# Performance work log

Hardware: AMD Instinct MI355X
Metric: run time of the kernel (lower is better)

## Reference

```python
import jax, jax.numpy as jnp
import numpy as np

D = 64
NU = 30000
NI = 20000
LU = 50  # mailbox length at user nodes (item_max_length)
LI = 50  # mailbox length at item nodes (user_max_length)


def setup_inputs() -> dict:
    key = jax.random.key(0)
    ks = jax.random.split(key, 14)
    s = 0.05
    return {
        "user_feat": jax.random.normal(ks[0], (NU, D), jnp.float32),
        "item_feat": jax.random.normal(ks[1], (NI, D), jnp.float32),
        "W_u": jax.random.normal(ks[2], (D, D), jnp.float32) * s,
        "W_i": jax.random.normal(ks[3], (D, D), jnp.float32) * s,
        "Wg_u": jax.random.normal(ks[4], (2 * D, D), jnp.float32) * s,
        "Wg_i": jax.random.normal(ks[5], (2 * D, D), jnp.float32) * s,
        "i_te": jax.random.normal(ks[6], (LI, D), jnp.float32) * s,
        "i_te_k": jax.random.normal(ks[7], (LI, D), jnp.float32) * s,
        "u_te": jax.random.normal(ks[8], (LU, D), jnp.float32) * s,
        "u_te_k": jax.random.normal(ks[9], (LU, D), jnp.float32) * s,
        "item_nbr": jax.random.randint(ks[10], (NI, LI), 0, NU, jnp.int32),
        "item_time": jax.random.randint(ks[11], (NI, LI), 0, 1000000, jnp.int32),
        "user_nbr": jax.random.randint(ks[12], (NU, LU), 0, NI, jnp.int32),
        "user_time": jax.random.randint(ks[13], (NU, LU), 0, 1000000, jnp.int32),
    }


def _orgat_att(src_mb, dst_h, time, te, te_k):
    """One DGSR reduce: long-term time-encoded attention + short-term last-attention.
    src_mb: [N, L, d] gathered source features; dst_h: [N, d]; time: [N, L] int.
    Returns concat([h_long, h_short]) @ Wg applied by caller.
    """
    L = time.shape[1]
    d = src_mb.shape[-1]
    scale = jnp.sqrt(jnp.asarray(d, src_mb.dtype))
    # rank of each edge's time within the neighborhood; re_order: 0 = most recent
    rank = jnp.argsort(jnp.argsort(time, axis=1), axis=1)
    re_o = L - rank - 1                                       # [N, L]
    e = jnp.sum((te[re_o] + src_mb) * dst_h[:, None, :], axis=2) / scale
    alpha = jax.nn.softmax(e, axis=1)                         # [N, L]
    h_long = jnp.sum(alpha[..., None] * (src_mb + te_k[re_o]), axis=1)
    # short-term: attention keyed on the most-recent neighbor
    last = jnp.argmax(time, axis=1)
    last_em = jnp.take_along_axis(src_mb, last[:, None, None], axis=1)  # [N,1,d]
    e1 = jnp.sum(last_em * src_mb, axis=2) / scale
    a1 = jax.nn.softmax(e1, axis=1)
    h_short = jnp.sum(a1[..., None] * src_mb, axis=1)
    return jnp.concatenate([h_long, h_short], axis=-1)        # [N, 2d]


def reference(user_feat, item_feat, W_u, W_i, Wg_u, Wg_i, i_te, i_te_k,
              u_te, u_te_k, item_nbr, item_time, user_nbr, user_time):
    uh = user_feat @ W_u   # user_weight (feat_drop=0)
    ih = item_feat @ W_i   # item_weight
    # 'by' edges: users -> items (item reduce uses user mailboxes + i_time_encoding)
    u_mb = uh[item_nbr]                                        # [NI, LI, d]
    item_new = _orgat_att(u_mb, ih, item_time, i_te, i_te_k) @ Wg_i
    # 'pby' edges: items -> users (user reduce uses item mailboxes + u_time_encoding)
    i_mb = ih[user_nbr]                                        # [NU, LU, d]
    user_new = _orgat_att(i_mb, uh, user_time, u_te, u_te_k) @ Wg_u
    # residual update functions
    user_out = jax.nn.elu(user_new + user_feat)
    item_out = jax.nn.elu(item_new + item_feat)
    return user_out, item_out
```

## Files before the change

kernel.cpp:

```cpp
#include <hip/hip_runtime.h>
#include <stdint.h>

#define D   64
#define L   50
#define NUM_U 30000
#define NUM_I 20000
#define PW  1976


typedef __attribute__((ext_vector_type(8))) short short8x;
typedef __attribute__((ext_vector_type(4))) float f32x4;

__device__ __forceinline__ float lof(unsigned int u) {
    union { unsigned int i; float f; } v; v.i = u << 16; return v.f;
}
__device__ __forceinline__ float hif(unsigned int u) {
    union { unsigned int i; float f; } v; v.i = u & 0xffff0000u; return v.f;
}
__device__ __forceinline__ unsigned int f2bfbits(float f) {
    union { float f; unsigned int i; } v; v.f = f;
    return (v.i + 0x7fffu + ((v.i >> 16) & 1u)) >> 16;
}
__device__ __forceinline__ unsigned int packbf(float a, float b) {
    return f2bfbits(a) | (f2bfbits(b) << 16);
}
__device__ __forceinline__ float rl(float v, int l) {
    return __int_as_float(__builtin_amdgcn_readlane(__float_as_int(v), l));
}
__device__ __forceinline__ int rli(int v, int l) {
    return __builtin_amdgcn_readlane(v, l);
}

__global__ __launch_bounds__(256) void prep(
    const float* __restrict__ user_feat, const float* __restrict__ item_feat,
    const float* __restrict__ W_u, const float* __restrict__ W_i,
    const float* __restrict__ Wg_i, const float* __restrict__ Wg_u,
    const float* __restrict__ te_i, const float* __restrict__ te_u,
    const float* __restrict__ tk_i, const float* __restrict__ tk_u,
    unsigned int* __restrict__ H,
    unsigned short* __restrict__ WgPi, unsigned short* __restrict__ WgPu,
    unsigned short* __restrict__ tePi, unsigned short* __restrict__ tePu,
    unsigned short* __restrict__ tkPi, unsigned short* __restrict__ tkPu)
{
    const int tid = threadIdx.x;
    if (blockIdx.x < 3125) {
        const int lane = tid & 63, wid = tid >> 6;
        int r0 = blockIdx.x * 16 + wid * 4;
        const float* src; const float* W;
        if (r0 < NUM_U) { src = user_feat + (size_t)r0 * D;            W = W_u; }
        else            { src = item_feat + (size_t)(r0 - NUM_U) * D;  W = W_i; }
        float f0 = src[0 * D + lane], f1 = src[1 * D + lane];
        float f2 = src[2 * D + lane], f3 = src[3 * D + lane];
        float a0 = 0.f, a1 = 0.f, a2 = 0.f, a3 = 0.f;
#pragma unroll
        for (int k = 0; k < 64; k++) {
            float wk = W[k * 64 + lane];
            a0 += rl(f0, k) * wk; a1 += rl(f1, k) * wk;
            a2 += rl(f2, k) * wk; a3 += rl(f3, k) * wk;
        }
        int li = (lane & 31) << 1;
        float p0 = __shfl(a0, li), q0 = __shfl(a0, li | 1);
        float p1 = __shfl(a1, li), q1 = __shfl(a1, li | 1);
        float p2 = __shfl(a2, li), q2 = __shfl(a2, li | 1);
        float p3 = __shfl(a3, li), q3 = __shfl(a3, li | 1);
        if (lane < 32) {
            H[(size_t)(r0 + 0) * 32 + lane] = packbf(p0, q0);
            H[(size_t)(r0 + 1) * 32 + lane] = packbf(p1, q1);
            H[(size_t)(r0 + 2) * 32 + lane] = packbf(p2, q2);
            H[(size_t)(r0 + 3) * 32 + lane] = packbf(p3, q3);
        }
    } else {
        int gid = (blockIdx.x - 3125) * 256 + tid;
        for (int idx = gid; idx < 8192; idx += 4096) {
            int n = idx >> 7, k = idx & 127;
            WgPi[idx] = (unsigned short)f2bfbits(Wg_i[k * 64 + n]);
            WgPu[idx] = (unsigned short)f2bfbits(Wg_u[k * 64 + n]);
        }
        {
            int idx = gid;
            int r = idx >> 6, k = idx & 63;
            tePi[idx] = (r < L) ? (unsigned short)f2bfbits(te_i[r * 64 + k]) : 0;
            tePu[idx] = (r < L) ? (unsigned short)f2bfbits(te_u[r * 64 + k]) : 0;
            int d = idx >> 6, rr = idx & 63;
            tkPi[idx] = (rr < L) ? (unsigned short)f2bfbits(tk_i[rr * 64 + d]) : 0;
            tkPu[idx] = (rr < L) ? (unsigned short)f2bfbits(tk_u[rr * 64 + d]) : 0;
        }
    }
}

__global__ __launch_bounds__(256, 5) void attn_fused(
    const unsigned int* __restrict__ H,
    const float* __restrict__ user_feat, const float* __restrict__ item_feat,
    const unsigned short* __restrict__ WgPi, const unsigned short* __restrict__ WgPu,
    const unsigned short* __restrict__ tePi, const unsigned short* __restrict__ tePu,
    const unsigned short* __restrict__ tkPi, const unsigned short* __restrict__ tkPu,
    const int* __restrict__ item_nbr, const int* __restrict__ item_time,
    const int* __restrict__ user_nbr, const int* __restrict__ user_time,
    float* __restrict__ out)
{
    __shared__ unsigned int lds[4 * PW];

    const int tid = threadIdx.x, lane = tid & 63, wid = tid >> 6;
    const bool iside = blockIdx.x < (NUM_I / 4);
    const int bb = iside ? blockIdx.x : blockIdx.x - NUM_I / 4;
    const int n = bb * 4 + wid;
    const int src_base = iside ? 0 : NUM_U;
    const int dst_base = iside ? NUM_U : 0;
    const float* dst_feat = iside ? item_feat : user_feat;
    const unsigned short* WgP  = iside ? WgPi : WgPu;
    const unsigned short* teP  = iside ? tePi : tePu;
    const unsigned short* tekP = iside ? tkPi : tkPu;
    const int* nbr   = iside ? item_nbr  : user_nbr;
    const int* timev = iside ? item_time : user_time;
    float* outp = out + (iside ? (size_t)NUM_U * D : 0);

    const int q4 = lane >> 4, c16 = lane & 15;

    unsigned int*   wld    = lds + wid * PW;
    unsigned int*   mbw    = wld;
    unsigned short* mbw_sh = (unsigned short*)mbw;
    float*          escf   = (float*)(wld + 1684);
    unsigned short* cat    = (unsigned short*)(wld + 1684);
    unsigned short* dla    = (unsigned short*)(wld + 1876);

    if (lane < 33) mbw[1650 + lane] = 0;

    int t   = (lane < L) ? timev[(size_t)n * L + lane] : 0;
    int nbv = (lane < L) ? nbr[(size_t)n * L + lane]  : 0;
    unsigned int key  = (lane < L) ? ((((unsigned)t) << 6) | (unsigned)lane) : 0u;
    unsigned int key2 = (lane < L) ? ((((unsigned)t) << 6) | (unsigned)(63 - lane)) : 0u;

    int rank = 0;
#pragma unroll
    for (int j = 0; j < L; j++) {
        unsigned int kj = (unsigned int)rli((int)key, j);
        rank += (kj < key) ? 1 : 0;
    }
    int re_o = (lane < L) ? (L - 1 - rank) : lane;

    unsigned int m2 = key2;
#pragma unroll
    for (int s = 32; s; s >>= 1) { unsigned int o2 = __shfl_xor(m2, s); m2 = (o2 > m2) ? o2 : m2; }
    const int last = 63 - (int)(m2 & 63u);

    unsigned int ud = H[(size_t)(dst_base + n) * 32 + (lane >> 1)];
    float dh = (lane & 1) ? hif(ud) : lof(ud);
    dla[lane] = (unsigned short)f2bfbits(dh);

    {
        const unsigned int* Hs = H + (size_t)src_base * 32;
        int half = lane >> 5, col = lane & 31;
#pragma unroll
        for (int l = 0; l < L; l += 2) {
            int ra = rli(nbv, l), rb = rli(nbv, l + 1);
            int r = half ? rb : ra;
            mbw[(l + half) * 33 + col] = Hs[(size_t)r * 32 + col];
        }
    }

    unsigned int ulm = mbw[last * 33 + (lane >> 1)];
    float lm = (lane & 1) ? hif(ulm) : lof(ulm);
    dla[64 + lane] = (unsigned short)f2bfbits(lm);

    f32x4 zero4 = {0.f, 0.f, 0.f, 0.f};
    f32x4 acc_e[4], acc_t[4];
#pragma unroll
    for (int nt = 0; nt < 4; nt++) { acc_e[nt] = zero4; acc_t[nt] = zero4; }
#pragma unroll
    for (int kt = 0; kt < 2; kt++) {
        short8x afr = *(const short8x*)(dla + (c16 & 1) * 64 + kt * 32 + q4 * 8);
#pragma unroll
        for (int nt = 0; nt < 4; nt++) {
            int row = c16 + 16 * nt;
            int rowc = (row > 50) ? 50 : row;
            union { short8x v; unsigned int u[4]; } bu;
            int base = rowc * 33 + kt * 16 + q4 * 4;
            bu.u[0] = mbw[base + 0]; bu.u[1] = mbw[base + 1];
            bu.u[2] = mbw[base + 2]; bu.u[3] = mbw[base + 3];
            acc_e[nt] = __builtin_amdgcn_mfma_f32_16x16x32_bf16(afr, bu.v, acc_e[nt], 0, 0, 0);
            short8x bt = *(const short8x*)(teP + row * 64 + kt * 32 + q4 * 8);
            acc_t[nt] = __builtin_amdgcn_mfma_f32_16x16x32_bf16(afr, bt, acc_t[nt], 0, 0, 0);
        }
    }
    if (q4 == 0) {
#pragma unroll
        for (int nt = 0; nt < 4; nt++) {
            escf[c16 + 16 * nt]       = acc_e[nt][0];
            escf[64 + c16 + 16 * nt]  = acc_e[nt][1];
            escf[128 + c16 + 16 * nt] = acc_t[nt][0];
        }
    }
    float e  = escf[lane];
    float e1 = escf[64 + lane];
    float th = escf[128 + re_o];

    e = (e + th) * 0.125f;
    e1 *= 0.125f;
    if (lane >= L) { e = -3e38f; e1 = -3e38f; }

    float mx = e;
#pragma unroll
    for (int s = 32; s; s >>= 1) { float o2 = __shfl_xor(mx, s); mx = (o2 > mx) ? o2 : mx; }
    float ex = __expf(e - mx);
    float sm = ex;
#pragma unroll
    for (int s = 32; s; s >>= 1) sm += __shfl_xor(sm, s);
    float alpha = ex / sm;

    float mx1 = e1;
#pragma unroll
    for (int s = 32; s; s >>= 1) { float o2 = __shfl_xor(mx1, s); mx1 = (o2 > mx1) ? o2 : mx1; }
    float ex1 = __expf(e1 - mx1);
    float sm1 = ex1;
#pragma unroll
    for (int s = 32; s; s >>= 1) sm1 += __shfl_xor(sm1, s);
    float aw = ex1 / sm1;

    dla[lane]       = (unsigned short)f2bfbits(alpha);
    dla[64 + lane]  = (unsigned short)f2bfbits(aw);
    dla[128 + re_o] = (unsigned short)f2bfbits(alpha);

    f32x4 acc_s[4], acc_k[4];
#pragma unroll
    for (int nt = 0; nt < 4; nt++) { acc_s[nt] = zero4; acc_k[nt] = zero4; }
#pragma unroll
    for (int kt = 0; kt < 2; kt++) {
        short8x aS = *(const short8x*)(dla + (c16 & 1) * 64 + kt * 32 + q4 * 8);
        short8x aB = *(const short8x*)(dla + 128 + kt * 32 + q4 * 8);
#pragma unroll
        for (int nt = 0; nt < 4; nt++) {
            int dcol = c16 + 16 * nt;
            short8x bM;
            if (kt == 0) {
                int b0 = (q4 * 8) * 66 + dcol;
#pragma unroll
                for (int i = 0; i < 8; i++) bM[i] = (short)mbw_sh[b0 + i * 66];
            } else {
#pragma unroll
                for (int i = 0; i < 8; i++) {
                    int k = 32 + q4 * 8 + i;
                    int kk = (k < L) ? k : 50;
                    bM[i] = (short)mbw_sh[kk * 66 + dcol];
                }
            }
            acc_s[nt] = __builtin_amdgcn_mfma_f32_16x16x32_bf16(aS, bM, acc_s[nt], 0, 0, 0);
            short8x bK = *(const short8x*)(tekP + dcol * 64 + kt * 32 + q4 * 8);
            acc_k[nt] = __builtin_amdgcn_mfma_f32_16x16x32_bf16(aB, bK, acc_k[nt], 0, 0, 0);
        }
    }
    if (q4 == 0) {
#pragma unroll
        for (int nt = 0; nt < 4; nt++) {
            cat[c16 + 16 * nt]      = (unsigned short)f2bfbits(acc_s[nt][0] + acc_k[nt][0]);
            cat[64 + c16 + 16 * nt] = (unsigned short)f2bfbits(acc_s[nt][1]);
        }
    }
    __syncthreads();

    short8x bfr[4];
#pragma unroll
    for (int tK = 0; tK < 4; tK++)
        bfr[tK] = *(const short8x*)(WgP + (wid * 16 + c16) * 128 + tK * 32 + q4 * 8);

    const unsigned short* catw = (const unsigned short*)(lds + (lane & 3) * PW + 1684);
    f32x4 acc = zero4;
#pragma unroll
    for (int tK = 0; tK < 4; tK++) {
        short8x a = *(const short8x*)(catw + tK * 32 + q4 * 8);
        acc = __builtin_amdgcn_mfma_f32_16x16x32_bf16(a, bfr[tK], acc, 0, 0, 0);
    }
    float r01 = (q4 & 1) ? acc[1] : acc[0];
    float r23 = (q4 & 1) ? acc[3] : acc[2];
    float pv  = (q4 & 2) ? r23 : r01;

    int node = bb * 4 + q4;
    float fres = dst_feat[(size_t)node * D + wid * 16 + c16];
    float oo = pv + fres;
    oo = (oo > 0.f) ? oo : (__expf(oo) - 1.f);
    outp[(size_t)node * D + wid * 16 + c16] = oo;
}

__global__ __launch_bounds__(256) void attn_mono(
    const float* __restrict__ src_feat, const float* __restrict__ dst_feat,
    const float* __restrict__ W_src, const float* __restrict__ W_dst,
    const float* __restrict__ Wg, const float* __restrict__ te,
    const float* __restrict__ tek, const int* __restrict__ nbr,
    const int* __restrict__ timev, float* __restrict__ out)
{
    __shared__ unsigned int ws32[64 * 33];
    __shared__ unsigned int te32[L * 33];
    __shared__ unsigned int mbs[4][L * 33];
    const int tid = threadIdx.x, lane = tid & 63, wid = tid >> 6;
    const int n = blockIdx.x * 4 + wid;
    {
        const float2* Wf2 = (const float2*)W_src;
        const float2* Te2 = (const float2*)te;
        for (int idx = tid; idx < 2048; idx += 256) {
            float2 w = Wf2[idx];
            ws32[(idx >> 5) * 33 + (idx & 31)] = packbf(w.x, w.y);
            if (idx < 1600) {
                float2 t2 = Te2[idx];
                te32[(idx >> 5) * 33 + (idx & 31)] = packbf(t2.x, t2.y);
            }
        }
    }
    __syncthreads();
    int t  = (lane < L) ? timev[(size_t)n * L + lane] : 0;
    int nb = (lane < L) ? nbr[(size_t)n * L + lane]  : 0;
    unsigned int key  = (lane < L) ? ((((unsigned)t) << 6) | (unsigned)lane) : 0u;
    unsigned int key2 = (lane < L) ? ((((unsigned)t) << 6) | (unsigned)(63 - lane)) : 0u;
    int rank = 0;
#pragma unroll
    for (int j = 0; j < L; j++) {
        unsigned int kj = (unsigned int)rli((int)key, j);
        rank += (kj < key) ? 1 : 0;
    }
    int re_o = (lane < L) ? (L - 1 - rank) : 0;
    unsigned int m2 = key2;
#pragma unroll
    for (int s = 32; s; s >>= 1) { unsigned int o2 = __shfl_xor(m2, s); m2 = (o2 > m2) ? o2 : m2; }
    const int last = 63 - (int)(m2 & 63u);
    const int rr = (lane < L) ? lane : (L - 1);
    float f = dst_feat[(size_t)n * D + lane];
    float dh;
    {
        float b0 = 0.f, b1 = 0.f, b2 = 0.f, b3 = 0.f;
#pragma unroll
        for (int k = 0; k < 64; k += 4) {
            b0 += rl(f, k + 0) * W_dst[(k + 0) * 64 + lane];
            b1 += rl(f, k + 1) * W_dst[(k + 1) * 64 + lane];
            b2 += rl(f, k + 2) * W_dst[(k + 2) * 64 + lane];
            b3 += rl(f, k + 3) * W_dst[(k + 3) * 64 + lane];
        }
        dh = (b0 + b1) + (b2 + b3);
    }
    float v1;
    {
        float b0 = 0.f, b1 = 0.f, b2 = 0.f, b3 = 0.f;
#pragma unroll
        for (int j = 0; j < 32; j += 2) {
            unsigned int u0 = ws32[lane * 33 + j];
            unsigned int u1 = ws32[lane * 33 + j + 1];
            b0 += lof(u0) * rl(dh, 2 * j + 0);
            b1 += hif(u0) * rl(dh, 2 * j + 1);
            b2 += lof(u1) * rl(dh, 2 * j + 2);
            b3 += hif(u1) * rl(dh, 2 * j + 3);
        }
        v1 = (b0 + b1) + (b2 + b3);
    }
    unsigned int* mbw = mbs[wid];
    {
        const float2* src2 = (const float2*)src_feat;
        int half = lane >> 5, col = lane & 31;
#pragma unroll
        for (int l = 0; l < L; l += 2) {
            int ra = rli(nb, l), rb = rli(nb, l + 1);
            int r = half ? rb : ra;
            float2 v = src2[(size_t)r * 32 + col];
            mbw[(l + half) * 33 + col] = packbf(v.x, v.y);
        }
    }
    __syncthreads();
    unsigned int ul = mbw[last * 33 + (lane >> 1)];
    float rlast = (lane & 1) ? hif(ul) : lof(ul);
    float g;
    {
        float b0 = 0.f, b1 = 0.f, b2 = 0.f, b3 = 0.f;
#pragma unroll
        for (int k = 0; k < 64; k += 4) {
            b0 += rl(rlast, k + 0) * W_src[(k + 0) * 64 + lane];
            b1 += rl(rlast, k + 1) * W_src[(k + 1) * 64 + lane];
            b2 += rl(rlast, k + 2) * W_src[(k + 2) * 64 + lane];
            b3 += rl(rlast, k + 3) * W_src[(k + 3) * 64 + lane];
        }
        g = (b0 + b1) + (b2 + b3);
    }
    float v2;
    {
        float b0 = 0.f, b1 = 0.f, b2 = 0.f, b3 = 0.f;
#pragma unroll
        for (int j = 0; j < 32; j += 2) {
            unsigned int u0 = ws32[lane * 33 + j];
            unsigned int u1 = ws32[lane * 33 + j + 1];
            b0 += lof(u0) * rl(g, 2 * j + 0);
            b1 += hif(u0) * rl(g, 2 * j + 1);
            b2 += lof(u1) * rl(g, 2 * j + 2);
            b3 += hif(u1) * rl(g, 2 * j + 3);
        }
        v2 = (b0 + b1) + (b2 + b3);
    }
    float teh;
    {
        float b0 = 0.f, b1 = 0.f, b2 = 0.f, b3 = 0.f;
#pragma unroll
        for (int j = 0; j < 32; j += 2) {
            unsigned int u0 = te32[rr * 33 + j];
            unsigned int u1 = te32[rr * 33 + j + 1];
            b0 += lof(u0) * rl(dh, 2 * j + 0);
            b1 += hif(u0) * rl(dh, 2 * j + 1);
            b2 += lof(u1) * rl(dh, 2 * j + 2);
            b3 += hif(u1) * rl(dh, 2 * j + 3);
        }
        teh = (b0 + b1) + (b2 + b3);
    }
    float e, e1;
    {
        float ea = 0.f, eb = 0.f, qa = 0.f, qb = 0.f;
#pragma unroll
        for (int j = 0; j < 32; j += 2) {
            unsigned int u0 = mbw[rr * 33 + j];
            unsigned int u1 = mbw[rr * 33 + j + 1];
            float m0 = lof(u0), m1 = hif(u0), m2f = lof(u1), m3 = hif(u1);
            ea += m0 * rl(v1, 2 * j + 0) + m1 * rl(v1, 2 * j + 1);
            eb += m2f * rl(v1, 2 * j + 2) + m3 * rl(v1, 2 * j + 3);
            qa += m0 * rl(v2, 2 * j + 0) + m1 * rl(v2, 2 * j + 1);
            qb += m2f * rl(v2, 2 * j + 2) + m3 * rl(v2, 2 * j + 3);
        }
        e = ea + eb; e1 = qa + qb;
    }
    e = (e + __shfl(teh, re_o)) * 0.125f;
    e1 *= 0.125f;
    if (lane >= L) { e = -3e38f; e1 = -3e38f; }
    float mx = e;
#pragma unroll
    for (int s = 32; s; s >>= 1) { float o2 = __shfl_xor(mx, s); mx = (o2 > mx) ? o2 : mx; }
    float ex = __expf(e - mx);
    float sm = ex;
#pragma unroll
    for (int s = 32; s; s >>= 1) sm += __shfl_xor(sm, s);
    float alpha = ex / sm;
    float mx1 = e1;
#pragma unroll
    for (int s = 32; s; s >>= 1) { float o2 = __shfl_xor(mx1, s); mx1 = (o2 > mx1) ? o2 : mx1; }
    float ex1 = __expf(e1 - mx1);
    float sm1 = ex1;
#pragma unroll
    for (int s = 32; s; s >>= 1) sm1 += __shfl_xor(sm1, s);
    float aw = ex1 / sm1;
    float sl, ss, tacc;
    {
        float sA = 0.f, sB = 0.f, hA = 0.f, hB = 0.f, tA = 0.f, tB = 0.f;
        int hcol = lane >> 1, odd = lane & 1;
#pragma unroll
        for (int l = 0; l < L; l += 2) {
            float saA = rl(alpha, l),     s1A = rl(aw, l);
            float saB = rl(alpha, l + 1), s1B = rl(aw, l + 1);
            int   roA = rli(re_o, l),     roB = rli(re_o, l + 1);
            unsigned int uA = mbw[(l + 0) * 33 + hcol];
            unsigned int uB = mbw[(l + 1) * 33 + hcol];
            float mA = odd ? hif(uA) : lof(uA);
            float mB = odd ? hif(uB) : lof(uB);
            sA += saA * mA; hA += s1A * mA; tA += saA * tek[roA * 64 + lane];
            sB += saB * mB; hB += s1B * mB; tB += saB * tek[roB * 64 + lane];
        }
        sl = sA + sB; ss = hA + hB; tacc = tA + tB;
    }
    float hl, hs;
    {
        float lA = 0.f, lB = 0.f, sA = 0.f, sB = 0.f;
#pragma unroll
        for (int k = 0; k < 64; k += 2) {
            float w0 = W_src[(k + 0) * 64 + lane];
            float w1 = W_src[(k + 1) * 64 + lane];
            lA += rl(sl, k + 0) * w0; sA += rl(ss, k + 0) * w0;
            lB += rl(sl, k + 1) * w1; sB += rl(ss, k + 1) * w1;
        }
        hl = tacc + lA + lB; hs = sA + sB;
    }
    float o;
    {
        float o0 = 0.f, o1 = 0.f, o2 = 0.f, o3 = 0.f;
#pragma unroll
        for (int k = 0; k < 64; k += 2) {
            o0 += rl(hl, k + 0) * Wg[(k + 0) * 64 + lane];
            o1 += rl(hl, k + 1) * Wg[(k + 1) * 64 + lane];
            o2 += rl(hs, k + 0) * Wg[(k + 64) * 64 + lane];
            o3 += rl(hs, k + 1) * Wg[(k + 65) * 64 + lane];
        }
        o = f + (o0 + o1) + (o2 + o3);
    }
    o = (o > 0.f) ? o : (__expf(o) - 1.f);
    out[(size_t)n * D + lane] = o;
}

extern "C" void kernel_launch(void* const* d_in, const int* in_sizes, int n_in,
                              void* d_out, int out_size, void* d_ws, size_t ws_size,
                              hipStream_t stream) {
    const float* user_feat = (const float*)d_in[0];
    const float* item_feat = (const float*)d_in[1];
    const float* W_u  = (const float*)d_in[2];
    const float* W_i  = (const float*)d_in[3];
    const float* Wg_u = (const float*)d_in[4];
    const float* Wg_i = (const float*)d_in[5];
    const float* i_te   = (const float*)d_in[6];
    const float* i_te_k = (const float*)d_in[7];
    const float* u_te   = (const float*)d_in[8];
    const float* u_te_k = (const float*)d_in[9];
    const int* item_nbr  = (const int*)d_in[10];
    const int* item_time = (const int*)d_in[11];
    const int* user_nbr  = (const int*)d_in[12];
    const int* user_time = (const int*)d_in[13];
    (void)in_sizes; (void)n_in; (void)out_size;

    float* outp = (float*)d_out;
    const size_t H_BYTES = (size_t)(NUM_U + NUM_I) * 32 * 4;
    const size_t NEED = H_BYTES + 2 * 16384 + 4 * 8192;

    if (ws_size >= NEED) {
        unsigned int* Hp = (unsigned int*)d_ws;
        unsigned char* aux = (unsigned char*)d_ws + H_BYTES;
        unsigned short* WgPi = (unsigned short*)(aux);
        unsigned short* WgPu = (unsigned short*)(aux + 16384);
        unsigned short* tePi = (unsigned short*)(aux + 32768);
        unsigned short* tePu = (unsigned short*)(aux + 40960);
        unsigned short* tkPi = (unsigned short*)(aux + 49152);
        unsigned short* tkPu = (unsigned short*)(aux + 57344);

        prep<<<3141, 256, 0, stream>>>(user_feat, item_feat, W_u, W_i,
                                       Wg_i, Wg_u, i_te, u_te, i_te_k, u_te_k,
                                       Hp, WgPi, WgPu, tePi, tePu, tkPi, tkPu);
        attn_fused<<<(NUM_I + NUM_U) / 4, 256, 0, stream>>>(
            Hp, user_feat, item_feat, WgPi, WgPu, tePi, tePu, tkPi, tkPu,
            item_nbr, item_time, user_nbr, user_time, outp);
    } else {
        attn_mono<<<NUM_I / 4, 256, 0, stream>>>(
            user_feat, item_feat, W_u, W_i, Wg_i, i_te, i_te_k,
            item_nbr, item_time, outp + (size_t)NUM_U * D);
        attn_mono<<<NUM_U / 4, 256, 0, stream>>>(
            item_feat, user_feat, W_i, W_u, Wg_u, u_te, u_te_k,
            user_nbr, user_time, outp);
    }
}
```

Measured before the change: 241.3 us.

## Read gathered mailbox rows directly from global instead of staging in LDS

The per-wave LDS staging of the 50-row gathered mailbox is removed. Both MFMA phases now fetch neighbor rows straight from the bf16 feature table, using row indices broadcast with ds_bpermute. The first phase loads 16-byte vectors, while the second phase does eight 2-byte scattered loads per operand. This shrinks LDS per block from about 31 KB to under 5 KB and raises the occupancy hint from 5 to 6 blocks, to remove the LDS write/read round trip and improve latency hiding. The cost is that every neighbor row is fetched twice from global/L2, and the transposed operand is built from many narrow loads.

```diff
diff --git a/kernel.cpp b/kernel.cpp
--- a/kernel.cpp
+++ b/kernel.cpp
@@ -5,7 +5,7 @@
 #define L   50
 #define NUM_U 30000
 #define NUM_I 20000
-#define PW  1976
+#define PW2 296
 
 
 typedef __attribute__((ext_vector_type(8))) short short8x;
@@ -88,7 +88,7 @@
     }
 }
 
-__global__ __launch_bounds__(256, 5) void attn_fused(
+__global__ __launch_bounds__(256, 6) void attn_fused(
     const unsigned int* __restrict__ H,
     const float* __restrict__ user_feat, const float* __restrict__ item_feat,
     const unsigned short* __restrict__ WgPi, const unsigned short* __restrict__ WgPu,
@@ -98,7 +98,7 @@
     const int* __restrict__ user_nbr, const int* __restrict__ user_time,
     float* __restrict__ out)
 {
-    __shared__ unsigned int lds[4 * PW];
+    __shared__ unsigned int lds[4 * PW2];
 
     const int tid = threadIdx.x, lane = tid & 63, wid = tid >> 6;
     const bool iside = blockIdx.x < (NUM_I / 4);
@@ -116,14 +116,13 @@
 
     const int q4 = lane >> 4, c16 = lane & 15;
 
-    unsigned int*   wld    = lds + wid * PW;
-    unsigned int*   mbw    = wld;
-    unsigned short* mbw_sh = (unsigned short*)mbw;
-    float*          escf   = (float*)(wld + 1684);
-    unsigned short* cat    = (unsigned short*)(wld + 1684);
-    unsigned short* dla    = (unsigned short*)(wld + 1876);
-
-    if (lane < 33) mbw[1650 + lane] = 0;
+    const unsigned short* Hs16 = (const unsigned short*)H + (size_t)src_base * 64;
+    const unsigned short* Hd16 = (const unsigned short*)H + (size_t)dst_base * 64;
+
+    unsigned int*   wld  = lds + wid * PW2;
+    unsigned short* dla  = (unsigned short*)wld;
+    float*          escf = (float*)(wld + 96);
+    unsigned short* cat  = (unsigned short*)(wld + 96);
 
     int t   = (lane < L) ? timev[(size_t)n * L + lane] : 0;
     int nbv = (lane < L) ? nbr[(size_t)n * L + lane]  : 0;
@@ -143,24 +142,14 @@
     for (int s = 32; s; s >>= 1) { unsigned int o2 = __shfl_xor(m2, s); m2 = (o2 > m2) ? o2 : m2; }
     const int last = 63 - (int)(m2 & 63u);
 
-    unsigned int ud = H[(size_t)(dst_base + n) * 32 + (lane >> 1)];
-    float dh = (lane & 1) ? hif(ud) : lof(ud);
-    dla[lane] = (unsigned short)f2bfbits(dh);
-
-    {
-        const unsigned int* Hs = H + (size_t)src_base * 32;
-        int half = lane >> 5, col = lane & 31;
-#pragma unroll
-        for (int l = 0; l < L; l += 2) {
-            int ra = rli(nbv, l), rb = rli(nbv, l + 1);
-            int r = half ? rb : ra;
-            mbw[(l + half) * 33 + col] = Hs[(size_t)r * 32 + col];
-        }
-    }
-
-    unsigned int ulm = mbw[last * 33 + (lane >> 1)];
-    float lm = (lane & 1) ? hif(ulm) : lof(ulm);
-    dla[64 + lane] = (unsigned short)f2bfbits(lm);
+    dla[lane] = Hd16[(size_t)n * 64 + lane];
+    int nbl = __shfl(nbv, last);
+    dla[64 + lane] = Hs16[(size_t)(unsigned)nbl * 64 + lane];
+
+    int rowN[4];
+#pragma unroll
+    for (int nt = 0; nt < 4; nt++)
+        rowN[nt] = __builtin_amdgcn_ds_bpermute((c16 + 16 * nt) << 2, nbv);
 
     f32x4 zero4 = {0.f, 0.f, 0.f, 0.f};
     f32x4 acc_e[4], acc_t[4];
@@ -172,12 +161,9 @@
 #pragma unroll
         for (int nt = 0; nt < 4; nt++) {
             int row = c16 + 16 * nt;
-            int rowc = (row > 50) ? 50 : row;
-            union { short8x v; unsigned int u[4]; } bu;
-            int base = rowc * 33 + kt * 16 + q4 * 4;
-            bu.u[0] = mbw[base + 0]; bu.u[1] = mbw[base + 1];
-            bu.u[2] = mbw[base + 2]; bu.u[3] = mbw[base + 3];
-            acc_e[nt] = __builtin_amdgcn_mfma_f32_16x16x32_bf16(afr, bu.v, acc_e[nt], 0, 0, 0);
+            short8x bv = *(const short8x*)(Hs16 + (unsigned)rowN[nt] * 64u
+                                                + (unsigned)(kt * 32 + q4 * 8));
+            acc_e[nt] = __builtin_amdgcn_mfma_f32_16x16x32_bf16(afr, bv, acc_e[nt], 0, 0, 0);
             short8x bt = *(const short8x*)(teP + row * 64 + kt * 32 + q4 * 8);
             acc_t[nt] = __builtin_amdgcn_mfma_f32_16x16x32_bf16(afr, bt, acc_t[nt], 0, 0, 0);
         }
@@ -227,23 +213,18 @@
     for (int kt = 0; kt < 2; kt++) {
         short8x aS = *(const short8x*)(dla + (c16 & 1) * 64 + kt * 32 + q4 * 8);
         short8x aB = *(const short8x*)(dla + 128 + kt * 32 + q4 * 8);
+        int ro[8];
+#pragma unroll
+        for (int i = 0; i < 8; i++)
+            ro[i] = __builtin_amdgcn_ds_bpermute((kt * 32 + q4 * 8 + i) << 2, nbv);
 #pragma unroll
         for (int nt = 0; nt < 4; nt++) {
             int dcol = c16 + 16 * nt;
-            short8x bM;
-            if (kt == 0) {
-                int b0 = (q4 * 8) * 66 + dcol;
-#pragma unroll
-                for (int i = 0; i < 8; i++) bM[i] = (short)mbw_sh[b0 + i * 66];
-            } else {
-#pragma unroll
-                for (int i = 0; i < 8; i++) {
-                    int k = 32 + q4 * 8 + i;
-                    int kk = (k < L) ? k : 50;
-                    bM[i] = (short)mbw_sh[kk * 66 + dcol];
-                }
-            }
-            acc_s[nt] = __builtin_amdgcn_mfma_f32_16x16x32_bf16(aS, bM, acc_s[nt], 0, 0, 0);
+            union { short8x v; unsigned short u[8]; } bu;
+#pragma unroll
+            for (int i = 0; i < 8; i++)
+                bu.u[i] = Hs16[(unsigned)ro[i] * 64u + (unsigned)dcol];
+            acc_s[nt] = __builtin_amdgcn_mfma_f32_16x16x32_bf16(aS, bu.v, acc_s[nt], 0, 0, 0);
             short8x bK = *(const short8x*)(tekP + dcol * 64 + kt * 32 + q4 * 8);
             acc_k[nt] = __builtin_amdgcn_mfma_f32_16x16x32_bf16(aB, bK, acc_k[nt], 0, 0, 0);
         }
@@ -262,7 +243,7 @@
     for (int tK = 0; tK < 4; tK++)
         bfr[tK] = *(const short8x*)(WgP + (wid * 16 + c16) * 128 + tK * 32 + q4 * 8);
 
-    const unsigned short* catw = (const unsigned short*)(lds + (lane & 3) * PW + 1684);
+    const unsigned short* catw = (const unsigned short*)(lds + (lane & 3) * PW2 + 96);
     f32x4 acc = zero4;
 #pragma unroll
     for (int tK = 0; tK < 4; tK++) {
```

Measured after the change: 278.6 us. +15.5%, slower.
